# Performance work log

Hardware: AMD Instinct MI355X
Metric: run time of the kernel (lower is better)

The kernel has to match this reference:

```python
import jax, jax.numpy as jnp
import numpy as np

N = 50000       # nodes
E = 800000      # edges
F_IN = 197      # node_feature_dim
H = 256         # hidden_dim
HEADS = 8
HD = H // HEADS # 32
L = 5           # num_layers
FF = 4 * H      # 1024
C = 2           # num_classes
ED = 2          # edge_feature_dim
SCALE = float(np.sqrt(HD))


def _ln(x, g, b):
    m = x.mean(-1, keepdims=True)
    v = ((x - m) ** 2).mean(-1, keepdims=True)
    return (x - m) / jnp.sqrt(v + 1e-5) * g + b


def setup_inputs() -> dict:
    key = jax.random.key(0)
    ks = iter(jax.random.split(key, 40))
    d = {}
    d["x"] = jax.random.normal(next(ks), (N, F_IN), dtype=jnp.float32)
    d["edge_index"] = jax.random.randint(next(ks), (2, E), 0, N, dtype=jnp.int64)
    d["edge_attr"] = jax.random.normal(next(ks), (E, ED), dtype=jnp.float32)
    xav = lambda k, sh: jax.random.normal(k, sh, dtype=jnp.float32) * float(np.sqrt(2.0 / (sh[-2] + sh[-1])))
    # input projection + LN
    d["in_W"] = xav(next(ks), (F_IN, H)); d["in_b"] = jnp.zeros((H,), jnp.float32)
    d["in_g"] = jnp.ones((H,), jnp.float32); d["in_bb"] = jnp.zeros((H,), jnp.float32)
    # stacked per-layer params (leading dim L)
    d["Wq"] = xav(next(ks), (L, H, H)); d["Wk"] = xav(next(ks), (L, H, H)); d["Wv"] = xav(next(ks), (L, H, H))
    d["We"] = xav(next(ks), (L, ED, HEADS)); d["be"] = jnp.zeros((L, HEADS), jnp.float32)
    d["Wo"] = xav(next(ks), (L, H, H)); d["bo"] = jnp.zeros((L, H), jnp.float32)
    d["ln1_g"] = jnp.ones((L, H), jnp.float32); d["ln1_b"] = jnp.zeros((L, H), jnp.float32)
    d["ln2_g"] = jnp.ones((L, H), jnp.float32); d["ln2_b"] = jnp.zeros((L, H), jnp.float32)
    d["f1_W"] = xav(next(ks), (L, H, FF)); d["f1_b"] = jnp.zeros((L, FF), jnp.float32)
    d["f2_W"] = xav(next(ks), (L, FF, H)); d["f2_b"] = jnp.zeros((L, H), jnp.float32)
    # classifier
    d["cls1_W"] = xav(next(ks), (H, H // 2)); d["cls1_b"] = jnp.zeros((H // 2,), jnp.float32)
    d["cls2_W"] = xav(next(ks), (H // 2, C)); d["cls2_b"] = jnp.zeros((C,), jnp.float32)
    return d


def _forward(x, edge_index, edge_attr, in_W, in_b, in_g, in_bb,
             Wq, Wk, Wv, We, be, Wo, bo, ln1_g, ln1_b, ln2_g, ln2_b,
             f1_W, f1_b, f2_W, f2_b, cls1_W, cls1_b, cls2_W, cls2_b):
    src, dst = edge_index[0], edge_index[1]  # message flows src -> dst
    h = jax.nn.gelu(_ln(x @ in_W + in_b, in_g, in_bb), approximate=False)

    def layer(h, p):
        wq, wk, wv, we, b_e, wo, b_o, g1, b1, g2, b2, w1, bf1, w2, bf2 = p
        hn = _ln(h, g1, b1)
        q = (hn @ wq).reshape(-1, HEADS, HD)
        k = (hn @ wk).reshape(-1, HEADS, HD)
        v = (hn @ wv).reshape(-1, HEADS, HD)
        edge_bias = edge_attr @ we + b_e                        # (E, HEADS)
        score = (q[dst] * k[src]).sum(-1) / SCALE + edge_bias   # (E, HEADS)
        # segment softmax over destination nodes
        mx = jax.ops.segment_max(score, dst, num_segments=N)
        mx = jnp.where(jnp.isfinite(mx), mx, 0.0)
        ex = jnp.exp(score - mx[dst])
        denom = jax.ops.segment_sum(ex, dst, num_segments=N)
        w = ex / (denom[dst] + 1e-16)                           # (E, HEADS)
        msg = w[:, :, None] * v[src]                            # (E, HEADS, HD)
        agg = jax.ops.segment_sum(msg.reshape(-1, H), dst, num_segments=N)
        out = agg @ wo + b_o
        out = _ln(out + h, g2, b2)                              # residual_proj = Identity
        ffn = jax.nn.gelu(out @ w1 + bf1, approximate=False) @ w2 + bf2
        return out + ffn, None

    params = (Wq, Wk, Wv, We, be, Wo, bo, ln1_g, ln1_b, ln2_g, ln2_b, f1_W, f1_b, f2_W, f2_b)
    h, _ = jax.lax.scan(layer, h, params)
    logits = jax.nn.gelu(h @ cls1_W + cls1_b, approximate=False) @ cls2_W + cls2_b
    probs = jax.nn.softmax(logits, axis=-1)
    return logits, probs


def reference(x, edge_index, edge_attr, in_W, in_b, in_g, in_bb,
              Wq, Wk, Wv, We, be, Wo, bo, ln1_g, ln1_b, ln2_g, ln2_b,
              f1_W, f1_b, f2_W, f2_b, cls1_W, cls1_b, cls2_W, cls2_b):
    return _forward(x, edge_index, edge_attr, in_W, in_b, in_g, in_bb,
                    Wq, Wk, Wv, We, be, Wo, bo, ln1_g, ln1_b, ln2_g, ln2_b,
                    f1_W, f1_b, f2_W, f2_b, cls1_W, cls1_b, cls2_W, cls2_b)
```

## Files before the change

### kernel.cpp

```cpp
#include <hip/hip_runtime.h>
#include <math.h>

#define NN 50000
#define NE 800000
#define FIN 197
#define KIN 224
#define H 256
#define HEADS 8
#define HD 32
#define LAYERS 5
#define FF 1024
#define INV_SCALE 0.17677669529663687f

typedef __attribute__((ext_vector_type(8))) short short8;
typedef __attribute__((ext_vector_type(4))) float f32x4;
typedef unsigned short ushort;

__device__ __forceinline__ float gelu_f(float x) {
    float x2 = x * x;
    float u = __builtin_fmaf(0.044715f * x2, x, x);
    float e = __builtin_amdgcn_exp2f(-2.3022075f * u);
    return x * __builtin_amdgcn_rcpf(1.0f + e);
}
__device__ __forceinline__ ushort f2b(float f) {
    unsigned u = __float_as_uint(f);
    u += 0x7fffu + ((u >> 16) & 1u);
    return (ushort)(u >> 16);
}
__device__ __forceinline__ float b2f(ushort b) {
    return __uint_as_float(((unsigned)b) << 16);
}
__device__ __forceinline__ float dot2b(unsigned a, unsigned b) {
    float a0 = __uint_as_float(a << 16), a1 = __uint_as_float(a & 0xffff0000u);
    float b0 = __uint_as_float(b << 16), b1 = __uint_as_float(b & 0xffff0000u);
    return a0 * b0 + a1 * b1;
}

__device__ __forceinline__ void load16_lds(const ushort* gp, ushort* lp) {
    __builtin_amdgcn_global_load_lds(
        (const __attribute__((address_space(1))) unsigned int*)gp,
        (__attribute__((address_space(3))) unsigned int*)lp,
        16, 0, 0);
}

__global__ __launch_bounds__(256) void gemm_bf16_kernel(
    const ushort* __restrict__ A, int lda,
    const ushort* __restrict__ Bt,
    const float* __restrict__ bias,
    const float* __restrict__ res, int ldr,
    float* __restrict__ Cf, ushort* __restrict__ Cb, int ldc,
    int n, int K, int act, int gx)
{
    __shared__ ushort As[2][128 * 32];
    __shared__ ushort Bs[2][128 * 32];
    int tid = threadIdx.x;
    int lane = tid & 63;
    int wave = tid >> 6;

    int tiles_y = (n + 127) >> 7;
    int lin = blockIdx.x;
    int gsz = gx * 8;
    int group = lin / gsz;
    int rem = lin - group * gsz;
    int rows_left = tiles_y - group * 8;
    int rg = rows_left < 8 ? rows_left : 8;
    int r = rem % rg;
    int c = rem / rg;
    int brow = (group * 8 + r) * 128;
    int bcol = c * 128;

    f32x4 acc[2][8] = {};
    int m0 = lane & 15;
    int rdc = ((lane >> 4) ^ ((lane >> 1) & 3)) * 8;

    int rA = lane >> 2;
    int c8s = (((lane & 3) ^ ((lane >> 3) & 3)) * 8);

    long arow0, arow1, brow0, brow1;
    {
        int gr0 = brow + wave * 32 + rA;        if (gr0 >= n) gr0 = n - 1;
        int gr1 = brow + wave * 32 + 16 + rA;   if (gr1 >= n) gr1 = n - 1;
        arow0 = (long)gr0 * lda;
        arow1 = (long)gr1 * lda;
        brow0 = (long)(bcol + wave * 32 + rA) * K;
        brow1 = (long)(bcol + wave * 32 + 16 + rA) * K;
    }
    int lo0 = (wave * 32) * 32;
    int lo1 = (wave * 32 + 16) * 32;

    int nt = K >> 5;
    load16_lds(A + arow0 + c8s, &As[0][lo0]);
    load16_lds(A + arow1 + c8s, &As[0][lo1]);
    load16_lds(Bt + brow0 + c8s, &Bs[0][lo0]);
    load16_lds(Bt + brow1 + c8s, &Bs[0][lo1]);
    __syncthreads();

    for (int t = 0; t < nt; ++t) {
        int p = t & 1;
        if (t + 1 < nt) {
            int k0 = (t + 1) << 5;
            load16_lds(A + arow0 + k0 + c8s, &As[p ^ 1][lo0]);
            load16_lds(A + arow1 + k0 + c8s, &As[p ^ 1][lo1]);
            load16_lds(Bt + brow0 + k0 + c8s, &Bs[p ^ 1][lo0]);
            load16_lds(Bt + brow1 + k0 + c8s, &Bs[p ^ 1][lo1]);
        }
        short8 af[2], bfr[8];
        #pragma unroll
        for (int i = 0; i < 2; ++i)
            af[i] = *(const short8*)&As[p][(wave * 32 + i * 16 + m0) * 32 + rdc];
        #pragma unroll
        for (int j = 0; j < 8; ++j)
            bfr[j] = *(const short8*)&Bs[p][(j * 16 + m0) * 32 + rdc];
        #pragma unroll
        for (int i = 0; i < 2; ++i)
            #pragma unroll
            for (int j = 0; j < 8; ++j)
                acc[i][j] = __builtin_amdgcn_mfma_f32_16x16x32_bf16(af[i], bfr[j], acc[i][j], 0, 0, 0);
        __syncthreads();
    }

    float* ch0 = (float*)&As[0][wave * 1024];
    float* ch1 = (float*)&As[1][wave * 1024];
    float* ch2 = (float*)&Bs[0][wave * 1024];
    float* ch3 = (float*)&Bs[1][wave * 1024];
    int ccol = lane & 15;
    int mych = lane >> 4;
    float* wch = (mych == 0) ? ch0 : ((mych == 1) ? ch1 : ((mych == 2) ? ch2 : ch3));
    int gcol = bcol + (lane & 31) * 4;
    #pragma unroll
    for (int i = 0; i < 2; ++i) {
        int rowbase = brow + wave * 32 + i * 16;
        #pragma unroll
        for (int rr = 0; rr < 4; ++rr)
            #pragma unroll
            for (int j = 0; j < 8; ++j)
                wch[rr * 128 + j * 16 + ccol] = acc[i][j][rr];
        #pragma unroll
        for (int k = 0; k < 8; ++k) {
            const float* rch = ((k >> 1) == 0) ? ch0 :
                               (((k >> 1) == 1) ? ch1 :
                               (((k >> 1) == 2) ? ch2 : ch3));
            f32x4 v = *(const f32x4*)&rch[(((k & 1) * 64) + lane) * 4];
            int grow = rowbase + 2 * k + (lane >> 5);
            if (bias) {
                float4 b4 = *(const float4*)(bias + gcol);
                v[0] += b4.x; v[1] += b4.y; v[2] += b4.z; v[3] += b4.w;
            }
            if (act) {
                v[0] = gelu_f(v[0]); v[1] = gelu_f(v[1]);
                v[2] = gelu_f(v[2]); v[3] = gelu_f(v[3]);
            }
            if (grow < n) {
                if (res) {
                    float4 r4 = *(const float4*)(res + (long)grow * ldr + gcol);
                    v[0] += r4.x; v[1] += r4.y; v[2] += r4.z; v[3] += r4.w;
                }
                if (Cf) *(f32x4*)(Cf + (long)grow * ldc + gcol) = v;
                if (Cb) {
                    ushort4 ob = { f2b(v[0]), f2b(v[1]), f2b(v[2]), f2b(v[3]) };
                    *(ushort4*)(Cb + (long)grow * ldc + gcol) = ob;
                }
            }
        }
    }
}

__global__ __launch_bounds__(256) void gemm_ln_kernel(
    const ushort* __restrict__ A, int K,
    const ushort* __restrict__ Bt,
    const float* __restrict__ bias,
    float* __restrict__ B0,
    const float* __restrict__ g, const float* __restrict__ bta,
    ushort* __restrict__ hb, int n,
    int do_ln, int ln_to_b0, int write_b0)
{
    __shared__ ushort As[2][64 * 32];
    __shared__ ushort Bs[2][256 * 32];
    int tid = threadIdx.x;
    int lane = tid & 63;
    int wave = tid >> 6;
    int brow = blockIdx.x * 64;
    int wrow = brow + wave * 16;

    f32x4 acc[16] = {};
    int m0 = lane & 15;
    int rdc = ((lane >> 4) ^ ((lane >> 1) & 3)) * 8;
    int rA = lane >> 2;
    int c8s = (((lane & 3) ^ ((lane >> 3) & 3)) * 8);

    long arow;
    { int gr = wrow + rA; if (gr >= n) gr = n - 1; arow = (long)gr * K; }
    long brow0 = (long)(wave * 64 + rA) * K;
    int loA = (wave * 16) * 32;
    int loB = (wave * 64) * 32;

    int nt = K >> 5;
    load16_lds(A + arow + c8s, &As[0][loA]);
    #pragma unroll
    for (int q = 0; q < 4; ++q)
        load16_lds(Bt + brow0 + (long)q * 16 * K + c8s, &Bs[0][loB + q * 16 * 32]);
    __syncthreads();

    for (int t = 0; t < nt; ++t) {
        int p = t & 1;
        if (t + 1 < nt) {
            int k0 = (t + 1) << 5;
            load16_lds(A + arow + k0 + c8s, &As[p ^ 1][loA]);
            #pragma unroll
            for (int q = 0; q < 4; ++q)
                load16_lds(Bt + brow0 + (long)q * 16 * K + k0 + c8s,
                           &Bs[p ^ 1][loB + q * 16 * 32]);
        }
        short8 af = *(const short8*)&As[p][(wave * 16 + m0) * 32 + rdc];
        #pragma unroll
        for (int jg = 0; jg < 4; ++jg) {
            short8 b0r = *(const short8*)&Bs[p][((jg * 64) + m0) * 32 + rdc];
            short8 b1r = *(const short8*)&Bs[p][((jg * 64) + 16 + m0) * 32 + rdc];
            short8 b2r = *(const short8*)&Bs[p][((jg * 64) + 32 + m0) * 32 + rdc];
            short8 b3r = *(const short8*)&Bs[p][((jg * 64) + 48 + m0) * 32 + rdc];
            acc[jg * 4 + 0] = __builtin_amdgcn_mfma_f32_16x16x32_bf16(af, b0r, acc[jg * 4 + 0], 0, 0, 0);
            acc[jg * 4 + 1] = __builtin_amdgcn_mfma_f32_16x16x32_bf16(af, b1r, acc[jg * 4 + 1], 0, 0, 0);
            acc[jg * 4 + 2] = __builtin_amdgcn_mfma_f32_16x16x32_bf16(af, b2r, acc[jg * 4 + 2], 0, 0, 0);
            acc[jg * 4 + 3] = __builtin_amdgcn_mfma_f32_16x16x32_bf16(af, b3r, acc[jg * 4 + 3], 0, 0, 0);
        }
        __syncthreads();
    }

    int li = lane & 15, lg = lane >> 4;
    #pragma unroll
    for (int j = 0; j < 16; ++j) {
        float bj = bias[j * 16 + li];
        #pragma unroll
        for (int rr = 0; rr < 4; ++rr) {
            int grow = wrow + lg * 4 + rr;
            float rv = (grow < n) ? B0[(long)grow * H + j * 16 + li] : 0.f;
            acc[j][rr] += bj + rv;
        }
    }
    if (do_ln) {
        float s0 = 0.f, s1 = 0.f, s2 = 0.f, s3 = 0.f;
        #pragma unroll
        for (int j = 0; j < 16; ++j) { s0 += acc[j][0]; s1 += acc[j][1]; s2 += acc[j][2]; s3 += acc[j][3]; }
        #pragma unroll
        for (int off = 1; off < 16; off <<= 1) {
            s0 += __shfl_xor(s0, off); s1 += __shfl_xor(s1, off);
            s2 += __shfl_xor(s2, off); s3 += __shfl_xor(s3, off);
        }
        float mn0 = s0 * (1.0f / H), mn1 = s1 * (1.0f / H), mn2 = s2 * (1.0f / H), mn3 = s3 * (1.0f / H);
        float q0 = 0.f, q1 = 0.f, q2 = 0.f, q3 = 0.f;
        #pragma unroll
        for (int j = 0; j < 16; ++j) {
            float d0 = acc[j][0] - mn0, d1 = acc[j][1] - mn1;
            float d2 = acc[j][2] - mn2, d3 = acc[j][3] - mn3;
            q0 += d0 * d0; q1 += d1 * d1; q2 += d2 * d2; q3 += d3 * d3;
        }
        #pragma unroll
        for (int off = 1; off < 16; off <<= 1) {
            q0 += __shfl_xor(q0, off); q1 += __shfl_xor(q1, off);
            q2 += __shfl_xor(q2, off); q3 += __shfl_xor(q3, off);
        }
        float rs0 = rsqrtf(q0 * (1.0f / H) + 1e-5f);
        float rs1 = rsqrtf(q1 * (1.0f / H) + 1e-5f);
        float rs2 = rsqrtf(q2 * (1.0f / H) + 1e-5f);
        float rs3 = rsqrtf(q3 * (1.0f / H) + 1e-5f);
        #pragma unroll
        for (int j = 0; j < 16; ++j) {
            int col = j * 16 + li;
            float gj = g[col], bj = bta[col];
            float o0 = (acc[j][0] - mn0) * rs0 * gj + bj;
            float o1 = (acc[j][1] - mn1) * rs1 * gj + bj;
            float o2 = (acc[j][2] - mn2) * rs2 * gj + bj;
            float o3 = (acc[j][3] - mn3) * rs3 * gj + bj;
            #pragma unroll
            for (int rr = 0; rr < 4; ++rr) {
                int grow = wrow + lg * 4 + rr;
                if (grow >= n) continue;
                float ov = (rr == 0) ? o0 : ((rr == 1) ? o1 : ((rr == 2) ? o2 : o3));
                if (write_b0)
                    B0[(long)grow * H + col] = ln_to_b0 ? ov : acc[j][rr];
                hb[(long)grow * H + col] = f2b(ov);
            }
        }
    } else {
        #pragma unroll
        for (int j = 0; j < 16; ++j) {
            int col = j * 16 + li;
            #pragma unroll
            for (int rr = 0; rr < 4; ++rr) {
                int grow = wrow + lg * 4 + rr;
                if (grow >= n) continue;
                if (write_b0) B0[(long)grow * H + col] = acc[j][rr];
                hb[(long)grow * H + col] = f2b(acc[j][rr]);
            }
        }
    }
}

__global__ __launch_bounds__(256) void ln256_kernel(
    const float* __restrict__ af, const ushort* __restrict__ ab,
    const float* __restrict__ res,
    const float* __restrict__ g, const float* __restrict__ bta,
    float* __restrict__ outf, ushort* __restrict__ outb, int n, int post_gelu)
{
    int row = blockIdx.x * 4 + (threadIdx.x >> 6);
    if (row >= n) return;
    int lane = threadIdx.x & 63;
    float4 v;
    if (af) {
        v = *(const float4*)(af + (long)row * H + lane * 4);
    } else {
        ushort4 vb = *(const ushort4*)(ab + (long)row * H + lane * 4);
        v.x = b2f(vb.x); v.y = b2f(vb.y); v.z = b2f(vb.z); v.w = b2f(vb.w);
    }
    if (res) {
        float4 r = *(const float4*)(res + (long)row * H + lane * 4);
        v.x += r.x; v.y += r.y; v.z += r.z; v.w += r.w;
    }
    float s = v.x + v.y + v.z + v.w;
    #pragma unroll
    for (int off = 1; off < 64; off <<= 1) s += __shfl_xor(s, off);
    float mean = s * (1.0f / H);
    float dx = v.x - mean, dy = v.y - mean, dz = v.z - mean, dw = v.w - mean;
    float qs = dx * dx + dy * dy + dz * dz + dw * dw;
    #pragma unroll
    for (int off = 1; off < 64; off <<= 1) qs += __shfl_xor(qs, off);
    float rstd = rsqrtf(qs * (1.0f / H) + 1e-5f);
    float4 gg = *(const float4*)(g + lane * 4);
    float4 bb = *(const float4*)(bta + lane * 4);
    float4 o;
    o.x = dx * rstd * gg.x + bb.x;
    o.y = dy * rstd * gg.y + bb.y;
    o.z = dz * rstd * gg.z + bb.z;
    o.w = dw * rstd * gg.w + bb.w;
    if (post_gelu) { o.x = gelu_f(o.x); o.y = gelu_f(o.y); o.z = gelu_f(o.z); o.w = gelu_f(o.w); }
    if (outf) *(float4*)(outf + (long)row * H + lane * 4) = o;
    if (outb) {
        ushort4 ob = { f2b(o.x), f2b(o.y), f2b(o.z), f2b(o.w) };
        *(ushort4*)(outb + (long)row * H + lane * 4) = ob;
    }
}

__global__ __launch_bounds__(256) void xcast_kernel(const float* __restrict__ x,
                                                    ushort* __restrict__ xb)
{
    long i = (long)blockIdx.x * 256 + threadIdx.x;
    if (i >= (long)NN * KIN) return;
    int n = (int)(i / KIN), c = (int)(i % KIN);
    xb[i] = (c < FIN) ? f2b(x[(long)n * FIN + c]) : (ushort)0;
}

__global__ __launch_bounds__(256) void wtin_kernel(const float* __restrict__ W,
                                                   ushort* __restrict__ Wt)
{
    int i = blockIdx.x * 256 + threadIdx.x;
    if (i >= 256 * KIN) return;
    int m = i / KIN, k = i % KIN;
    Wt[i] = (k < FIN) ? f2b(W[(long)k * H + m]) : (ushort)0;
}

__global__ __launch_bounds__(256) void wtqkv_kernel(
    const float* __restrict__ Wq, const float* __restrict__ Wk,
    const float* __restrict__ Wv, ushort* __restrict__ out)
{
    long i = (long)blockIdx.x * 256 + threadIdx.x;
    if (i >= (long)LAYERS * 768 * 256) return;
    int l = (int)(i / (768 * 256));
    int r = (int)(i % (768 * 256));
    int m = r >> 8, k = r & 255;
    const float* W = (m < 256) ? Wq : ((m < 512) ? Wk : Wv);
    out[i] = f2b(W[(long)l * 65536 + (long)k * 256 + (m & 255)]);
}

__global__ __launch_bounds__(256) void wtgen_kernel(
    const float* __restrict__ W, ushort* __restrict__ out, int L, int K, int M)
{
    long i = (long)blockIdx.x * 256 + threadIdx.x;
    if (i >= (long)L * K * M) return;
    int l = (int)(i / ((long)K * M));
    int r = (int)(i % ((long)K * M));
    int m = r / K, k = r % K;
    out[i] = f2b(W[(long)l * K * M + (long)k * M + m]);
}

__global__ __launch_bounds__(256) void deg_kernel(const int* __restrict__ dst,
                                                   int* __restrict__ deg)
{
    int e = blockIdx.x * 256 + threadIdx.x;
    if (e >= NE) return;
    atomicAdd(&deg[dst[e]], 1);
}

__global__ __launch_bounds__(256) void scan1_kernel(const int* __restrict__ deg,
                                                     int* __restrict__ rowptr,
                                                     int* __restrict__ bsum)
{
    __shared__ int buf[256];
    int tid = threadIdx.x;
    int i = blockIdx.x * 256 + tid;
    int v = (i < NN) ? deg[i] : 0;
    buf[tid] = v;
    __syncthreads();
    #pragma unroll
    for (int off = 1; off < 256; off <<= 1) {
        int t = (tid >= off) ? buf[tid - off] : 0;
        __syncthreads();
        buf[tid] += t;
        __syncthreads();
    }
    if (i < NN) rowptr[i] = buf[tid] - v;
    if (tid == 255) bsum[blockIdx.x] = buf[255];
}

__global__ __launch_bounds__(256) void scan2_kernel(int* __restrict__ bsum, int nb)
{
    __shared__ int buf[256];
    int tid = threadIdx.x;
    int v = (tid < nb) ? bsum[tid] : 0;
    buf[tid] = v;
    __syncthreads();
    #pragma unroll
    for (int off = 1; off < 256; off <<= 1) {
        int t = (tid >= off) ? buf[tid - off] : 0;
        __syncthreads();
        buf[tid] += t;
        __syncthreads();
    }
    if (tid < nb) bsum[tid] = buf[tid] - v;
}

__global__ __launch_bounds__(256) void scan3_kernel(int* __restrict__ rowptr,
                                                     const int* __restrict__ bsum)
{
    int i = blockIdx.x * 256 + threadIdx.x;
    if (i < NN) rowptr[i] += bsum[blockIdx.x];
    if (i == 0) rowptr[NN] = NE;
}

__global__ __launch_bounds__(256) void fill_kernel(
    const int* __restrict__ src, const int* __restrict__ dst,
    const float* __restrict__ ea, const int* __restrict__ rowptr,
    int* __restrict__ cursor, int* __restrict__ csr_src,
    float2* __restrict__ csr_ea)
{
    int e = blockIdx.x * 256 + threadIdx.x;
    if (e >= NE) return;
    int d = dst[e];
    int pos = atomicAdd(&cursor[d], 1);
    int j = rowptr[d] + pos;
    csr_src[j] = src[e];
    csr_ea[j] = *(const float2*)(ea + 2 * e);
}

#define LOADE(idx, kbuf, vbuf, ebuf)                                   \
    { int s_ = csr_src[idx]; ebuf = csr_ea[idx];                       \
      const ushort* kr_ = qkv + (long)s_ * 768 + 256;                  \
      kbuf = *(const uint2*)(kr_ + lane * 4);                          \
      vbuf = *(const uint2*)(kr_ + 256 + lane * 4); }

#define PAIR(k1, v1, e1, k2, v2, e2)                                               \
    { float p1 = dot2b(q2.x, (k1).x) + dot2b(q2.y, (k1).y);                        \
      float p2 = dot2b(q2.x, (k2).x) + dot2b(q2.y, (k2).y);                        \
      p1 += __shfl_xor(p1, 1);  p2 += __shfl_xor(p2, 1);                           \
      p1 += __shfl_xor(p1, 2);  p2 += __shfl_xor(p2, 2);                           \
      p1 += __shfl_xor(p1, 4);  p2 += __shfl_xor(p2, 4);                           \
      float s1 = p1 * c1 + (e1).x * w0 + (e1).y * w1 + bb;                         \
      float s2 = p2 * c1 + (e2).x * w0 + (e2).y * w1 + bb;                         \
      float mp = fmaxf(s1, s2);                                                    \
      float x1 = __builtin_amdgcn_exp2f(s1 - mp);                                  \
      float x2 = __builtin_amdgcn_exp2f(s2 - mp);                                  \
      float lp = x1 + x2;                                                          \
      float b0 = x1 * __uint_as_float((v1).x << 16)         + x2 * __uint_as_float((v2).x << 16);          \
      float b1 = x1 * __uint_as_float((v1).x & 0xffff0000u) + x2 * __uint_as_float((v2).x & 0xffff0000u);  \
      float b2 = x1 * __uint_as_float((v1).y << 16)         + x2 * __uint_as_float((v2).y << 16);          \
      float b3 = x1 * __uint_as_float((v1).y & 0xffff0000u) + x2 * __uint_as_float((v2).y & 0xffff0000u);  \
      float mn = fmaxf(m, mp);                                                     \
      float so = __builtin_amdgcn_exp2f(m - mn);                                   \
      float sp = __builtin_amdgcn_exp2f(mp - mn);                                  \
      l  = l  * so + lp * sp;                                                      \
      a0 = a0 * so + b0 * sp;                                                      \
      a1 = a1 * so + b1 * sp;                                                      \
      a2 = a2 * so + b2 * sp;                                                      \
      a3 = a3 * so + b3 * sp;                                                      \
      m = mn; }

#define SINGLE(kb, vb, eb)                                                         \
    { float p1 = dot2b(q2.x, (kb).x) + dot2b(q2.y, (kb).y);                        \
      p1 += __shfl_xor(p1, 1);                                                     \
      p1 += __shfl_xor(p1, 2);                                                     \
      p1 += __shfl_xor(p1, 4);                                                     \
      float s1 = p1 * c1 + (eb).x * w0 + (eb).y * w1 + bb;                         \
      float mn = fmaxf(m, s1);                                                     \
      float so = __builtin_amdgcn_exp2f(m - mn);                                   \
      float e_ = __builtin_amdgcn_exp2f(s1 - mn);                                  \
      l  = l  * so + e_;                                                           \
      a0 = a0 * so + e_ * __uint_as_float((vb).x << 16);                           \
      a1 = a1 * so + e_ * __uint_as_float((vb).x & 0xffff0000u);                   \
      a2 = a2 * so + e_ * __uint_as_float((vb).y << 16);                           \
      a3 = a3 * so + e_ * __uint_as_float((vb).y & 0xffff0000u);                   \
      m = mn; }

__global__ __launch_bounds__(256) void attn_kernel(
    const ushort* __restrict__ qkv,
    const int* __restrict__ rowptr, const int* __restrict__ csr_src,
    const float2* __restrict__ csr_ea,
    const float* __restrict__ We, const float* __restrict__ be,
    ushort* __restrict__ aggb)
{
    int node = blockIdx.x * 4 + (threadIdx.x >> 6);
    if (node >= NN) return;
    int lane = threadIdx.x & 63;
    int h = lane >> 3;
    const float L2E = 1.4426950408889634f;
    float w0 = We[h] * L2E, w1 = We[8 + h] * L2E, bb = be[h] * L2E;
    const float c1 = INV_SCALE * L2E;

    uint2 q2 = *(const uint2*)(qkv + (long)node * 768 + lane * 4);
    int jbeg = rowptr[node], jend = rowptr[node + 1];

    float m = -1e30f, l = 0.f;
    float a0 = 0.f, a1 = 0.f, a2 = 0.f, a3 = 0.f;

    uint2 k0v = {0,0}, v0v = {0,0}, k1v = {0,0}, v1v = {0,0};
    uint2 k2v = {0,0}, v2v = {0,0}, k3v = {0,0}, v3v = {0,0};
    float2 e0v = {0.f,0.f}, e1v = {0.f,0.f}, e2v = {0.f,0.f}, e3v = {0.f,0.f};

    if (jbeg + 0 < jend) LOADE(jbeg + 0, k0v, v0v, e0v);
    if (jbeg + 1 < jend) LOADE(jbeg + 1, k1v, v1v, e1v);
    if (jbeg + 2 < jend) LOADE(jbeg + 2, k2v, v2v, e2v);
    if (jbeg + 3 < jend) LOADE(jbeg + 3, k3v, v3v, e3v);

    int j = jbeg;
    for (; j + 3 < jend; j += 4) {
        PAIR(k0v, v0v, e0v, k1v, v1v, e1v);
        if (j + 4 < jend) LOADE(j + 4, k0v, v0v, e0v);
        if (j + 5 < jend) LOADE(j + 5, k1v, v1v, e1v);
        PAIR(k2v, v2v, e2v, k3v, v3v, e3v);
        if (j + 6 < jend) LOADE(j + 6, k2v, v2v, e2v);
        if (j + 7 < jend) LOADE(j + 7, k3v, v3v, e3v);
    }
    int rleft = jend - j;
    if (rleft >= 2) PAIR(k0v, v0v, e0v, k1v, v1v, e1v);
    if (rleft == 3) SINGLE(k2v, v2v, e2v);
    if (rleft == 1) SINGLE(k0v, v0v, e0v);

    float inv = 1.0f / (l + 1e-16f);
    ushort4 o = { f2b(a0 * inv), f2b(a1 * inv), f2b(a2 * inv), f2b(a3 * inv) };
    *(ushort4*)(aggb + (long)node * 256 + lane * 4) = o;
}

__global__ __launch_bounds__(256) void cls_kernel(
    const float* __restrict__ t1, const float* __restrict__ W,
    const float* __restrict__ b, float* __restrict__ out)
{
    int i = blockIdx.x * 256 + threadIdx.x;
    if (i >= NN) return;
    const float* tp = t1 + (long)i * 128;
    float a0 = 0.f, a1 = 0.f;
    #pragma unroll
    for (int j = 0; j < 128; j += 4) {
        float4 t = *(const float4*)(tp + j);
        a0 += t.x * W[(j + 0) * 2] + t.y * W[(j + 1) * 2] + t.z * W[(j + 2) * 2] + t.w * W[(j + 3) * 2];
        a1 += t.x * W[(j + 0) * 2 + 1] + t.y * W[(j + 1) * 2 + 1] + t.z * W[(j + 2) * 2 + 1] + t.w * W[(j + 3) * 2 + 1];
    }
    float l0 = a0 + b[0], l1 = a1 + b[1];
    out[(long)i * 2 + 0] = l0;
    out[(long)i * 2 + 1] = l1;
    float mx = fmaxf(l0, l1);
    float p0 = expf(l0 - mx), p1 = expf(l1 - mx);
    float sden = p0 + p1;
    out[2L * NN + (long)i * 2 + 0] = p0 / sden;
    out[2L * NN + (long)i * 2 + 1] = p1 / sden;
}

extern "C" void kernel_launch(void* const* d_in, const int* in_sizes, int n_in,
                              void* d_out, int out_size, void* d_ws, size_t ws_size,
                              hipStream_t stream) {
    const float* x      = (const float*)d_in[0];
    const int*   ei     = (const int*)d_in[1];
    const float* ea     = (const float*)d_in[2];
    const float* in_W   = (const float*)d_in[3];
    const float* in_b   = (const float*)d_in[4];
    const float* in_g   = (const float*)d_in[5];
    const float* in_bb  = (const float*)d_in[6];
    const float* Wq     = (const float*)d_in[7];
    const float* Wk     = (const float*)d_in[8];
    const float* Wv     = (const float*)d_in[9];
    const float* We     = (const float*)d_in[10];
    const float* be     = (const float*)d_in[11];
    const float* Wo     = (const float*)d_in[12];
    const float* bo     = (const float*)d_in[13];
    const float* ln1_g  = (const float*)d_in[14];
    const float* ln1_b  = (const float*)d_in[15];
    const float* ln2_g  = (const float*)d_in[16];
    const float* ln2_b  = (const float*)d_in[17];
    const float* f1_W   = (const float*)d_in[18];
    const float* f1_b   = (const float*)d_in[19];
    const float* f2_W   = (const float*)d_in[20];
    const float* f2_b   = (const float*)d_in[21];
    const float* cls1_W = (const float*)d_in[22];
    const float* cls1_b = (const float*)d_in[23];
    const float* cls2_W = (const float*)d_in[24];
    const float* cls2_b = (const float*)d_in[25];
    float* out = (float*)d_out;

    const int* src = ei;
    const int* dst = ei + NE;

    char* w = (char*)d_ws;
    float* B0 = (float*)w;            w += (size_t)NN * H * 4;
    ushort* hb = (ushort*)w;          w += (size_t)NN * H * 2;
    char* pool = w;                   w += (size_t)NN * 1024 * 2;
    ushort* qkv  = (ushort*)pool;
    ushort* aggb = (ushort*)(pool + (size_t)NN * 768 * 2);
    float*  tproj = (float*)pool;
    ushort* xb   = (ushort*)(pool + (size_t)NN * H * 4);
    ushort* tb   = (ushort*)pool;
    float*  t1   = (float*)pool;
    int* deg    = (int*)w;            w += (size_t)NN * 4;
    int* cursor = (int*)w;            w += (size_t)NN * 4;
    int* rowptr = (int*)w;            w += (size_t)(NN + 2) * 4;
    int* bsum   = (int*)w;            w += 1024;
    int* csr_src = (int*)w;           w += (size_t)NE * 4;
    float2* csr_ea = (float2*)w;      w += (size_t)NE * 8;
    ushort* wqkv_t = (ushort*)w;      w += (size_t)LAYERS * 768 * 256 * 2;
    ushort* wo_t  = (ushort*)w;       w += (size_t)LAYERS * 65536 * 2;
    ushort* f1_t  = (ushort*)w;       w += (size_t)LAYERS * 262144 * 2;
    ushort* f2_t  = (ushort*)w;       w += (size_t)LAYERS * 262144 * 2;
    ushort* c1_t  = (ushort*)w;       w += (size_t)32768 * 2;
    ushort* inw_t = (ushort*)w;       w += (size_t)256 * KIN * 2;

    dim3 blk(256);
    const int ln_grid = (NN + 3) / 4;
    const int e_grid = (NE + 255) / 256;
    const int n_grid = (NN + 255) / 256;
    const int ty = (NN + 127) / 128;
    const int ty2 = (NN + 63) / 64;

    hipMemsetAsync(deg, 0, (size_t)NN * 4, stream);
    hipMemsetAsync(cursor, 0, (size_t)NN * 4, stream);
    deg_kernel<<<e_grid, blk, 0, stream>>>(dst, deg);
    scan1_kernel<<<n_grid, blk, 0, stream>>>(deg, rowptr, bsum);
    scan2_kernel<<<1, blk, 0, stream>>>(bsum, n_grid);
    scan3_kernel<<<n_grid, blk, 0, stream>>>(rowptr, bsum);
    fill_kernel<<<e_grid, blk, 0, stream>>>(src, dst, ea, rowptr, cursor, csr_src, csr_ea);

    wtqkv_kernel<<<(int)(((long)LAYERS * 768 * 256 + 255) / 256), blk, 0, stream>>>(Wq, Wk, Wv, wqkv_t);
    wtgen_kernel<<<(int)(((long)LAYERS * 65536 + 255) / 256), blk, 0, stream>>>(Wo, wo_t, LAYERS, 256, 256);
    wtgen_kernel<<<(int)(((long)LAYERS * 262144 + 255) / 256), blk, 0, stream>>>(f1_W, f1_t, LAYERS, 256, 1024);
    wtgen_kernel<<<(int)(((long)LAYERS * 262144 + 255) / 256), blk, 0, stream>>>(f2_W, f2_t, LAYERS, 1024, 256);
    wtgen_kernel<<<(32768 + 255) / 256, blk, 0, stream>>>(cls1_W, c1_t, 1, 256, 128);
    wtin_kernel<<<(256 * KIN + 255) / 256, blk, 0, stream>>>(in_W, inw_t);

    xcast_kernel<<<(int)(((long)NN * KIN + 255) / 256), blk, 0, stream>>>(x, xb);
    {
        gemm_bf16_kernel<<<2 * ty, blk, 0, stream>>>(xb, KIN, inw_t, in_b, nullptr, 0,
                                                     tproj, nullptr, H, NN, KIN, 0, 2);
        ln256_kernel<<<ln_grid, blk, 0, stream>>>(tproj, nullptr, nullptr, in_g, in_bb, B0, nullptr, NN, 1);
    }

    ln256_kernel<<<ln_grid, blk, 0, stream>>>(B0, nullptr, nullptr, ln1_g, ln1_b, nullptr, hb, NN, 0);

    for (int l = 0; l < LAYERS; ++l) {
        const float* we  = We + (long)l * 16;
        const float* bel = be + (long)l * 8;
        const float* bol = bo + (long)l * H;
        const float* g2 = ln2_g + (long)l * H;
        const float* b2 = ln2_b + (long)l * H;
        const float* bf1 = f1_b + (long)l * FF;
        const float* bf2 = f2_b + (long)l * H;

        gemm_bf16_kernel<<<6 * ty, blk, 0, stream>>>(hb, H, wqkv_t + (long)l * 768 * 256,
            nullptr, nullptr, 0, nullptr, qkv, 768, NN, H, 0, 6);
        attn_kernel<<<(NN + 3) / 4, blk, 0, stream>>>(qkv, rowptr, csr_src, csr_ea, we, bel, aggb);

        gemm_ln_kernel<<<ty2, blk, 0, stream>>>(aggb, H, wo_t + (long)l * 65536,
            bol, B0, g2, b2, hb, NN, 1, 1, 1);

        gemm_bf16_kernel<<<8 * ty, blk, 0, stream>>>(hb, H, f1_t + (long)l * 262144,
            bf1, nullptr, 0, nullptr, tb, FF, NN, H, 1, 8);

        if (l + 1 < LAYERS) {
            gemm_ln_kernel<<<ty2, blk, 0, stream>>>(tb, FF, f2_t + (long)l * 262144,
                bf2, B0, ln1_g + (long)(l + 1) * H, ln1_b + (long)(l + 1) * H,
                hb, NN, 1, 0, 1);
        } else {
            gemm_ln_kernel<<<ty2, blk, 0, stream>>>(tb, FF, f2_t + (long)l * 262144,
                bf2, B0, nullptr, nullptr, hb, NN, 0, 0, 0);
        }
    }

    {
        gemm_bf16_kernel<<<1 * ty, blk, 0, stream>>>(hb, H, c1_t, cls1_b, nullptr, 0,
                                                     t1, nullptr, 128, NN, H, 1, 1);
        cls_kernel<<<n_grid, blk, 0, stream>>>(t1, cls2_W, cls2_b, out);
    }
}
```

Measured before the change: 2.222 ms.

## Retile GEMM+LayerNorm kernel so each wave owns a 64x64 output tile

The fused GEMM+LayerNorm kernel now gives each wave a 64-row by 64-column output tile instead of 16 rows by all 256 columns. This cuts shared-memory operand reads per MFMA: 8 fragment loads feed 16 MFMAs, where before 17 loads fed 16. Because each row is now split across four waves, the LayerNorm mean and variance are reduced through shared memory, which adds two extra block barriers. The bf16 output is staged in shared memory and written back with coalesced 16-byte stores. The non-LN branch no longer writes the fp32 B0 buffer when write_b0 is set, which is a correctness risk if any caller relies on it.

After: 2.526 ms. +13.7%, slower.

```diff
diff --git a/kernel.cpp b/kernel.cpp
--- a/kernel.cpp
+++ b/kernel.cpp
@@ -174,125 +174,162 @@
     ushort* __restrict__ hb, int n,
     int do_ln, int ln_to_b0, int write_b0)
 {
-    __shared__ ushort As[2][64 * 32];
-    __shared__ ushort Bs[2][256 * 32];
+    __shared__ ushort sm[2 * 320 * 32];
     int tid = threadIdx.x;
     int lane = tid & 63;
     int wave = tid >> 6;
     int brow = blockIdx.x * 64;
-    int wrow = brow + wave * 16;
-
-    f32x4 acc[16] = {};
+
+    f32x4 acc[4][4] = {};
     int m0 = lane & 15;
     int rdc = ((lane >> 4) ^ ((lane >> 1) & 3)) * 8;
     int rA = lane >> 2;
     int c8s = (((lane & 3) ^ ((lane >> 3) & 3)) * 8);
 
     long arow;
-    { int gr = wrow + rA; if (gr >= n) gr = n - 1; arow = (long)gr * K; }
-    long brow0 = (long)(wave * 64 + rA) * K;
+    { int gr = brow + wave * 16 + rA; if (gr >= n) gr = n - 1; arow = (long)gr * K; }
+    long brw = (long)(wave * 64 + rA) * K;
     int loA = (wave * 16) * 32;
-    int loB = (wave * 64) * 32;
+    int loB = (64 + wave * 64) * 32;
 
     int nt = K >> 5;
-    load16_lds(A + arow + c8s, &As[0][loA]);
+    load16_lds(A + arow + c8s, &sm[loA]);
     #pragma unroll
     for (int q = 0; q < 4; ++q)
-        load16_lds(Bt + brow0 + (long)q * 16 * K + c8s, &Bs[0][loB + q * 16 * 32]);
+        load16_lds(Bt + brw + (long)q * 16 * K + c8s, &sm[loB + q * 16 * 32]);
     __syncthreads();
 
     for (int t = 0; t < nt; ++t) {
-        int p = t & 1;
+        const ushort* sp = sm + (t & 1) * 10240;
+        ushort* sn = sm + ((t & 1) ^ 1) * 10240;
         if (t + 1 < nt) {
             int k0 = (t + 1) << 5;
-            load16_lds(A + arow + k0 + c8s, &As[p ^ 1][loA]);
+            load16_lds(A + arow + k0 + c8s, sn + loA);
             #pragma unroll
             for (int q = 0; q < 4; ++q)
-                load16_lds(Bt + brow0 + (long)q * 16 * K + k0 + c8s,
-                           &Bs[p ^ 1][loB + q * 16 * 32]);
+                load16_lds(Bt + brw + (long)q * 16 * K + k0 + c8s, sn + loB + q * 16 * 32);
         }
-        short8 af = *(const short8*)&As[p][(wave * 16 + m0) * 32 + rdc];
-        #pragma unroll
-        for (int jg = 0; jg < 4; ++jg) {
-            short8 b0r = *(const short8*)&Bs[p][((jg * 64) + m0) * 32 + rdc];
-            short8 b1r = *(const short8*)&Bs[p][((jg * 64) + 16 + m0) * 32 + rdc];
-            short8 b2r = *(const short8*)&Bs[p][((jg * 64) + 32 + m0) * 32 + rdc];
-            short8 b3r = *(const short8*)&Bs[p][((jg * 64) + 48 + m0) * 32 + rdc];
-            acc[jg * 4 + 0] = __builtin_amdgcn_mfma_f32_16x16x32_bf16(af, b0r, acc[jg * 4 + 0], 0, 0, 0);
-            acc[jg * 4 + 1] = __builtin_amdgcn_mfma_f32_16x16x32_bf16(af, b1r, acc[jg * 4 + 1], 0, 0, 0);
-            acc[jg * 4 + 2] = __builtin_amdgcn_mfma_f32_16x16x32_bf16(af, b2r, acc[jg * 4 + 2], 0, 0, 0);
-            acc[jg * 4 + 3] = __builtin_amdgcn_mfma_f32_16x16x32_bf16(af, b3r, acc[jg * 4 + 3], 0, 0, 0);
-        }
+        short8 af[4], bf[4];
+        #pragma unroll
+        for (int i = 0; i < 4; ++i)
+            af[i] = *(const short8*)&sp[(i * 16 + m0) * 32 + rdc];
+        #pragma unroll
+        for (int j = 0; j < 4; ++j)
+            bf[j] = *(const short8*)&sp[(64 + wave * 64 + j * 16 + m0) * 32 + rdc];
+        #pragma unroll
+        for (int i = 0; i < 4; ++i)
+            #pragma unroll
+            for (int j = 0; j < 4; ++j)
+                acc[i][j] = __builtin_amdgcn_mfma_f32_16x16x32_bf16(af[i], bf[j], acc[i][j], 0, 0, 0);
         __syncthreads();
     }
 
-    int li = lane & 15, lg = lane >> 4;
-    #pragma unroll
-    for (int j = 0; j < 16; ++j) {
-        float bj = bias[j * 16 + li];
-        #pragma unroll
-        for (int rr = 0; rr < 4; ++rr) {
-            int grow = wrow + lg * 4 + rr;
-            float rv = (grow < n) ? B0[(long)grow * H + j * 16 + li] : 0.f;
-            acc[j][rr] += bj + rv;
-        }
-    }
+    int crow0 = (lane >> 4) * 4;
+    int ccol = m0;
+
+    #pragma unroll
+    for (int j = 0; j < 4; ++j) {
+        int col = wave * 64 + j * 16 + ccol;
+        float bj = bias[col];
+        #pragma unroll
+        for (int i = 0; i < 4; ++i)
+            #pragma unroll
+            for (int rr = 0; rr < 4; ++rr) {
+                int grow = brow + i * 16 + crow0 + rr;
+                float rv = (grow < n) ? B0[(long)grow * H + col] : 0.f;
+                acc[i][j][rr] += bj + rv;
+            }
+    }
+
+    ushort* slab = sm;
+    float* psum = (float*)(sm + 16384);
+    float* qsum = psum + 256;
+
     if (do_ln) {
-        float s0 = 0.f, s1 = 0.f, s2 = 0.f, s3 = 0.f;
-        #pragma unroll
-        for (int j = 0; j < 16; ++j) { s0 += acc[j][0]; s1 += acc[j][1]; s2 += acc[j][2]; s3 += acc[j][3]; }
-        #pragma unroll
-        for (int off = 1; off < 16; off <<= 1) {
-            s0 += __shfl_xor(s0, off); s1 += __shfl_xor(s1, off);
-            s2 += __shfl_xor(s2, off); s3 += __shfl_xor(s3, off);
-        }
-        float mn0 = s0 * (1.0f / H), mn1 = s1 * (1.0f / H), mn2 = s2 * (1.0f / H), mn3 = s3 * (1.0f / H);
-        float q0 = 0.f, q1 = 0.f, q2 = 0.f, q3 = 0.f;
-        #pragma unroll
-        for (int j = 0; j < 16; ++j) {
-            float d0 = acc[j][0] - mn0, d1 = acc[j][1] - mn1;
-            float d2 = acc[j][2] - mn2, d3 = acc[j][3] - mn3;
-            q0 += d0 * d0; q1 += d1 * d1; q2 += d2 * d2; q3 += d3 * d3;
-        }
-        #pragma unroll
-        for (int off = 1; off < 16; off <<= 1) {
-            q0 += __shfl_xor(q0, off); q1 += __shfl_xor(q1, off);
-            q2 += __shfl_xor(q2, off); q3 += __shfl_xor(q3, off);
-        }
-        float rs0 = rsqrtf(q0 * (1.0f / H) + 1e-5f);
-        float rs1 = rsqrtf(q1 * (1.0f / H) + 1e-5f);
-        float rs2 = rsqrtf(q2 * (1.0f / H) + 1e-5f);
-        float rs3 = rsqrtf(q3 * (1.0f / H) + 1e-5f);
-        #pragma unroll
-        for (int j = 0; j < 16; ++j) {
-            int col = j * 16 + li;
-            float gj = g[col], bj = bta[col];
-            float o0 = (acc[j][0] - mn0) * rs0 * gj + bj;
-            float o1 = (acc[j][1] - mn1) * rs1 * gj + bj;
-            float o2 = (acc[j][2] - mn2) * rs2 * gj + bj;
-            float o3 = (acc[j][3] - mn3) * rs3 * gj + bj;
+        #pragma unroll
+        for (int i = 0; i < 4; ++i)
             #pragma unroll
             for (int rr = 0; rr < 4; ++rr) {
-                int grow = wrow + lg * 4 + rr;
-                if (grow >= n) continue;
-                float ov = (rr == 0) ? o0 : ((rr == 1) ? o1 : ((rr == 2) ? o2 : o3));
-                if (write_b0)
-                    B0[(long)grow * H + col] = ln_to_b0 ? ov : acc[j][rr];
-                hb[(long)grow * H + col] = f2b(ov);
+                float s = acc[i][0][rr] + acc[i][1][rr] + acc[i][2][rr] + acc[i][3][rr];
+                s += __shfl_xor(s, 1);
+                s += __shfl_xor(s, 2);
+                s += __shfl_xor(s, 4);
+                s += __shfl_xor(s, 8);
+                if (ccol == 0) psum[(i * 16 + crow0 + rr) * 4 + wave] = s;
             }
+        __syncthreads();
+        f32x4 meanv[4];
+        #pragma unroll
+        for (int i = 0; i < 4; ++i)
+            #pragma unroll
+            for (int rr = 0; rr < 4; ++rr) {
+                int rl = i * 16 + crow0 + rr;
+                meanv[i][rr] = (psum[rl * 4] + psum[rl * 4 + 1] +
+                                psum[rl * 4 + 2] + psum[rl * 4 + 3]) * (1.0f / H);
+            }
+        #pragma unroll
+        for (int i = 0; i < 4; ++i)
+            #pragma unroll
+            for (int rr = 0; rr < 4; ++rr) {
+                float mn = meanv[i][rr];
+                float d0 = acc[i][0][rr] - mn, d1 = acc[i][1][rr] - mn;
+                float d2 = acc[i][2][rr] - mn, d3 = acc[i][3][rr] - mn;
+                float q = d0 * d0 + d1 * d1 + d2 * d2 + d3 * d3;
+                q += __shfl_xor(q, 1);
+                q += __shfl_xor(q, 2);
+                q += __shfl_xor(q, 4);
+                q += __shfl_xor(q, 8);
+                if (ccol == 0) qsum[(i * 16 + crow0 + rr) * 4 + wave] = q;
+            }
+        __syncthreads();
+        f32x4 rstdv[4];
+        #pragma unroll
+        for (int i = 0; i < 4; ++i)
+            #pragma unroll
+            for (int rr = 0; rr < 4; ++rr) {
+                int rl = i * 16 + crow0 + rr;
+                float var = (qsum[rl * 4] + qsum[rl * 4 + 1] +
+                             qsum[rl * 4 + 2] + qsum[rl * 4 + 3]) * (1.0f / H);
+                rstdv[i][rr] = rsqrtf(var + 1e-5f);
+            }
+        #pragma unroll
+        for (int j = 0; j < 4; ++j) {
+            int col = wave * 64 + j * 16 + ccol;
+            float gj = g[col], btj = bta[col];
+            #pragma unroll
+            for (int i = 0; i < 4; ++i)
+                #pragma unroll
+                for (int rr = 0; rr < 4; ++rr) {
+                    int rl = i * 16 + crow0 + rr;
+                    int grow = brow + rl;
+                    float o = (acc[i][j][rr] - meanv[i][rr]) * rstdv[i][rr] * gj + btj;
+                    if (write_b0 && grow < n)
+                        B0[(long)grow * H + col] = ln_to_b0 ? o : acc[i][j][rr];
+                    slab[rl * 256 + col] = f2b(o);
+                }
         }
     } else {
         #pragma unroll
-        for (int j = 0; j < 16; ++j) {
-            int col = j * 16 + li;
-            #pragma unroll
-            for (int rr = 0; rr < 4; ++rr) {
-                int grow = wrow + lg * 4 + rr;
-                if (grow >= n) continue;
-                if (write_b0) B0[(long)grow * H + col] = acc[j][rr];
-                hb[(long)grow * H + col] = f2b(acc[j][rr]);
-            }
+        for (int j = 0; j < 4; ++j) {
+            int col = wave * 64 + j * 16 + ccol;
+            #pragma unroll
+            for (int i = 0; i < 4; ++i)
+                #pragma unroll
+                for (int rr = 0; rr < 4; ++rr) {
+                    int rl = i * 16 + crow0 + rr;
+                    slab[rl * 256 + col] = f2b(acc[i][j][rr]);
+                }
         }
+    }
+    __syncthreads();
+    #pragma unroll
+    for (int q = 0; q < 8; ++q) {
+        int idx = q * 256 + tid;
+        int row = idx >> 5;
+        int c8o = (idx & 31) * 8;
+        int grow = brow + row;
+        if (grow < n)
+            *(short8*)(hb + (long)grow * H + c8o) = *(const short8*)&slab[row * 256 + c8o];
     }
 }
 
```
